# Performance work log

Measured on AMD Instinct MI355X. Metric: run time of the kernel, lower is better.

The kernel has to match this reference:

```python
import jax, jax.numpy as jnp
import numpy as np

VNUM = 50000
OUT = 128
E = 1600000
EPS = 1e-7


def setup_inputs() -> dict:
    key = jax.random.key(0)
    k = jax.random.split(key, 8)
    sidx = jax.random.randint(k[0], (E,), 0, VNUM, dtype=jnp.int64 if jax.config.jax_enable_x64 else jnp.int32)
    tidx = jax.random.randint(k[1], (E,), 0, VNUM, dtype=sidx.dtype)
    enorm = jax.random.uniform(k[2], (E,), dtype=jnp.float32)
    # edge signs +-1 as in signed graph conv
    esgn = jnp.where(jax.random.uniform(k[3], (E,)) < 0.5, -1.0, 1.0).astype(jnp.float32)
    # vrepr initialized trunc_normal(std=0.1) (zero_init=False)
    vrepr = 0.1 * jax.random.truncated_normal(k[4], -2.0, 2.0, (VNUM, OUT), dtype=jnp.float32)
    lim = 1.0 / np.sqrt(OUT)
    loc_w = jax.random.uniform(k[5], (OUT, OUT), jnp.float32, -lim, lim)
    loc_b = jnp.zeros((OUT,), jnp.float32)
    std_w = jax.random.uniform(k[6], (OUT, OUT), jnp.float32, -lim, lim)
    std_b = jnp.zeros((OUT,), jnp.float32)
    return {"sidx": sidx, "tidx": tidx, "enorm": enorm, "esgn": esgn,
            "vrepr": vrepr, "loc_w": loc_w, "loc_b": loc_b,
            "std_w": std_w, "std_b": std_b}


def reference(sidx, tidx, enorm, esgn, vrepr, loc_w, loc_b, std_w, std_b):
    # GraphConv: edge-weighted gather + scatter-add aggregation
    msg = vrepr[sidx] * (esgn * enorm)[:, None]          # [E, OUT]
    ptr = jax.ops.segment_sum(msg, tidx, num_segments=VNUM)  # [VNUM, OUT]
    loc = ptr @ loc_w.T + loc_b                          # Normal loc
    std = jax.nn.softplus(ptr @ std_w.T + std_b) + EPS   # Normal scale
    return loc, std
```

## Files before the change

kernel.cpp:

```cpp
#include <hip/hip_runtime.h>
#include <math.h>

#define VNUM 50000
#define OUTF 128
#define NEDGE 1600000
#define EPSF 1e-7f

#define CONV_BLOCKS 6250
#define BFRAG_BLOCKS 64

#define CHUNK 2048
#define NCB 49
#define COARSE_BLOCKS 782

typedef __attribute__((ext_vector_type(8))) short short8;
typedef __attribute__((ext_vector_type(4))) float v4f;

__device__ __forceinline__ unsigned short f2bf(float f) {
    union { float f; unsigned int u; } c; c.f = f;
    unsigned int u = c.u;
    return (unsigned short)((u + 0x7FFFu + ((u >> 16) & 1u)) >> 16);
}
__device__ __forceinline__ float bf16_lo(unsigned int p) {
    union { unsigned int u; float f; } c; c.u = p << 16; return c.f;
}
__device__ __forceinline__ float bf16_hi(unsigned int p) {
    union { unsigned int u; float f; } c; c.u = p & 0xFFFF0000u; return c.f;
}

__device__ __forceinline__ int wave_incl_scan(int v, int lane) {
#pragma unroll
    for (int off = 1; off < 64; off <<= 1) {
        const int o = __shfl_up(v, off, 64);
        if (lane >= off) v += o;
    }
    return v;
}

__global__ __launch_bounds__(256) void prep_kernel(
    const float* __restrict__ vrepr, unsigned int* __restrict__ vrepr16,
    const int* __restrict__ tidx, int* __restrict__ chist,
    const float* __restrict__ loc_w, const float* __restrict__ std_w,
    unsigned int* bfrag)
{
    __shared__ int lc[4][NCB];
    const int b = blockIdx.x, tid = threadIdx.x;
    if (b < CONV_BLOCKS) {
        const size_t base = (size_t)b * 1024 + tid * 4;
        const float4 v = *reinterpret_cast<const float4*>(vrepr + base);
        uint2 o;
        o.x = (unsigned)f2bf(v.x) | ((unsigned)f2bf(v.y) << 16);
        o.y = (unsigned)f2bf(v.z) | ((unsigned)f2bf(v.w) << 16);
        *reinterpret_cast<uint2*>(vrepr16 + base / 2) = o;
    } else if (b < CONV_BLOCKS + COARSE_BLOCKS) {
        const int hb = b - CONV_BLOCKS;
        for (int i = tid; i < 4 * NCB; i += 256) (&lc[0][0])[i] = 0;
        __syncthreads();
        const int base = hb * CHUNK;
#pragma unroll
        for (int j = 0; j < 8; ++j) {
            const int e = base + j * 256 + tid;
            if (e < NEDGE) atomicAdd(&lc[tid >> 6][tidx[e] >> 10], 1);
        }
        __syncthreads();
        if (tid < NCB) {
            const int s = lc[0][tid] + lc[1][tid] + lc[2][tid] + lc[3][tid];
            if (s) atomicAdd(&chist[tid], s);
        }
    } else {
        const int p = (b - (CONV_BLOCKS + COARSE_BLOCKS)) * 256 + tid;
        const int j2 = p & 3, lq = (p >> 2) & 63, ks = (p >> 8) & 3, ct = p >> 10;
        const int k = ks * 32 + (lq >> 4) * 8 + j2 * 2;
        const int n = ct * 16 + (lq & 15);
        const float* wsrc = (n >> 7) ? std_w : loc_w;
        const int c = n & 127;
        bfrag[p] = (unsigned)f2bf(wsrc[c * 128 + k]) |
                   ((unsigned)f2bf(wsrc[c * 128 + k + 1]) << 16);
    }
}

__global__ __launch_bounds__(64) void scan_coarse_kernel(
    const int* __restrict__ chist, int* __restrict__ cbase,
    int* __restrict__ ccursor, int* __restrict__ offs)
{
    const int tid = threadIdx.x;
    const int v = (tid < NCB) ? chist[tid] : 0;
    const int inc = wave_incl_scan(v, tid);
    const int ex = inc - v;
    if (tid < NCB) { cbase[tid] = ex; ccursor[tid] = ex; }
    if (tid == NCB - 1) { cbase[NCB] = inc; offs[VNUM] = inc; }
}

__global__ __launch_bounds__(256) void coarse_kernel(
    const int* __restrict__ sidx, const int* __restrict__ tidx,
    const float* __restrict__ enorm, const float* __restrict__ esgn,
    int* __restrict__ ccursor, uint2* __restrict__ coarse8)
{
    __shared__ uint2 lrec[CHUNK];
    __shared__ int lcnt[4][NCB];
    __shared__ int lbase[4][NCB];
    __shared__ int loffs[NCB];
    __shared__ int grun[NCB];

    const int tid = threadIdx.x, lane = tid & 63, wv = tid >> 6;
    const int base = blockIdx.x * CHUNK;
    const int n = min(CHUNK, NEDGE - base);

    for (int i = tid; i < 4 * NCB; i += 256) (&lcnt[0][0])[i] = 0;
    __syncthreads();

    uint2 rec[8];
#pragma unroll
    for (int j = 0; j < 8; ++j) {
        const int e = base + j * 256 + tid;
        if (e < NEDGE) {
            const int t = tidx[e];
            const float w = esgn[e] * enorm[e];
            rec[j].x = ((unsigned)sidx[e] << 16) | (unsigned)f2bf(w);
            rec[j].y = (unsigned)t;
            atomicAdd(&lcnt[wv][t >> 10], 1);
        }
    }
    __syncthreads();

    if (tid < 64) {
        int c0 = 0, c1 = 0, c2 = 0, c3 = 0, tot = 0;
        if (lane < NCB) {
            c0 = lcnt[0][lane]; c1 = lcnt[1][lane];
            c2 = lcnt[2][lane]; c3 = lcnt[3][lane];
            tot = c0 + c1 + c2 + c3;
        }
        const int inc = wave_incl_scan(tot, lane);
        const int ex = inc - tot;
        if (lane < NCB) {
            loffs[lane]    = ex;
            lbase[0][lane] = ex;
            lbase[1][lane] = ex + c0;
            lbase[2][lane] = ex + c0 + c1;
            lbase[3][lane] = ex + c0 + c1 + c2;
            grun[lane] = atomicAdd(&ccursor[lane], tot);
        }
    }
    __syncthreads();

#pragma unroll
    for (int j = 0; j < 8; ++j) {
        const int e = base + j * 256 + tid;
        if (e < NEDGE) {
            const int cb = (int)(rec[j].y >> 10);
            const int pos = atomicAdd(&lbase[wv][cb], 1);
            lrec[pos] = rec[j];
        }
    }
    __syncthreads();

    for (int i = tid; i < n; i += 256) {
        const uint2 r = lrec[i];
        const int cb = (int)(r.y >> 10);
        coarse8[grun[cb] + (i - loffs[cb])] = r;
    }
}

__global__ __launch_bounds__(1024) void binsort_kernel(
    const uint2* __restrict__ coarse8, const int* __restrict__ cbase,
    int* __restrict__ offs, unsigned int* __restrict__ pairs)
{
    __shared__ int cnt[1024];
    __shared__ int cur[1024];
    __shared__ int wsum[16];
    const int tid = threadIdx.x, lane = tid & 63, wv = tid >> 6;
    const int bin = blockIdx.x;
    const int s0 = cbase[bin], e0 = cbase[bin + 1];

    cnt[tid] = 0;
    __syncthreads();
    for (int i = s0 + tid; i < e0; i += 1024)
        atomicAdd(&cnt[coarse8[i].y & 1023], 1);
    __syncthreads();

    const int v = cnt[tid];
    const int inc = wave_incl_scan(v, lane);
    if (lane == 63) wsum[wv] = inc;
    __syncthreads();
    if (tid == 0) {
        int run = 0;
        for (int i2 = 0; i2 < 16; ++i2) { const int t2 = wsum[i2]; wsum[i2] = run; run += t2; }
    }
    __syncthreads();
    const int ex = s0 + wsum[wv] + inc - v;
    const int gv = (bin << 10) + tid;
    if (gv < VNUM) offs[gv] = ex;
    cur[tid] = ex;
    __syncthreads();

    for (int i = s0 + tid; i < e0; i += 1024) {
        const uint2 r = coarse8[i];
        const int pos = atomicAdd(&cur[r.y & 1023], 1);
        pairs[pos] = r.x;
    }
}

__global__ __launch_bounds__(256) void aggregate_kernel(
    const int* __restrict__ offs, const unsigned int* __restrict__ pairs,
    const unsigned int* __restrict__ vrepr16, float* __restrict__ acc)
{
    const int v = blockIdx.x * 4 + (threadIdx.x >> 6);
    const int l = threadIdx.x & 63;
    int i = offs[v];
    const int end = offs[v + 1];

    float a0 = 0.0f, a1 = 0.0f;
    for (; i + 8 <= end; i += 8) {
        unsigned p[8], r[8];
#pragma unroll
        for (int j = 0; j < 8; ++j) p[j] = pairs[i + j];
#pragma unroll
        for (int j = 0; j < 8; ++j) r[j] = vrepr16[(size_t)(p[j] >> 16) * 64 + l];
#pragma unroll
        for (int j = 0; j < 8; ++j) {
            const float w = bf16_lo(p[j]);
            a0 = fmaf(bf16_lo(r[j]), w, a0);
            a1 = fmaf(bf16_hi(r[j]), w, a1);
        }
    }
    for (; i + 4 <= end; i += 4) {
        const unsigned p0 = pairs[i], p1 = pairs[i + 1];
        const unsigned p2 = pairs[i + 2], p3 = pairs[i + 3];
        const unsigned r0 = vrepr16[(size_t)(p0 >> 16) * 64 + l];
        const unsigned r1 = vrepr16[(size_t)(p1 >> 16) * 64 + l];
        const unsigned r2 = vrepr16[(size_t)(p2 >> 16) * 64 + l];
        const unsigned r3 = vrepr16[(size_t)(p3 >> 16) * 64 + l];
        const float w0 = bf16_lo(p0), w1 = bf16_lo(p1);
        const float w2 = bf16_lo(p2), w3 = bf16_lo(p3);
        a0 = fmaf(bf16_lo(r0), w0, a0); a1 = fmaf(bf16_hi(r0), w0, a1);
        a0 = fmaf(bf16_lo(r1), w1, a0); a1 = fmaf(bf16_hi(r1), w1, a1);
        a0 = fmaf(bf16_lo(r2), w2, a0); a1 = fmaf(bf16_hi(r2), w2, a1);
        a0 = fmaf(bf16_lo(r3), w3, a0); a1 = fmaf(bf16_hi(r3), w3, a1);
    }
    for (; i < end; ++i) {
        const unsigned p = pairs[i];
        const unsigned r = vrepr16[(size_t)(p >> 16) * 64 + l];
        const float w = bf16_lo(p);
        a0 = fmaf(bf16_lo(r), w, a0); a1 = fmaf(bf16_hi(r), w, a1);
    }
    *reinterpret_cast<float2*>(acc + (size_t)v * OUTF + 2 * l) = make_float2(a0, a1);
}

__global__ __launch_bounds__(256) void gemm_mfma_kernel(
    const float* acc, const unsigned int* __restrict__ bfrag,
    const float* __restrict__ loc_b, const float* __restrict__ std_b,
    float* out)
{
    __shared__ unsigned short tile[16][136];
    const int t = threadIdx.x;
    const int row0 = blockIdx.x * 16;
    const int l = t & 63, w = t >> 6;

    short8 bfr[4][4];
#pragma unroll
    for (int ct = 0; ct < 4; ++ct)
#pragma unroll
        for (int ks = 0; ks < 4; ++ks)
            bfr[ct][ks] = *reinterpret_cast<const short8*>(
                bfrag + ((((w * 4 + ct) * 4 + ks) * 64 + l) << 2));

    {
        const float* src = acc + (size_t)row0 * OUTF + t * 8;
        const float4 v0 = *reinterpret_cast<const float4*>(src);
        const float4 v1 = *reinterpret_cast<const float4*>(src + 4);
        uint4 pk;
        pk.x = (unsigned)f2bf(v0.x) | ((unsigned)f2bf(v0.y) << 16);
        pk.y = (unsigned)f2bf(v0.z) | ((unsigned)f2bf(v0.w) << 16);
        pk.z = (unsigned)f2bf(v1.x) | ((unsigned)f2bf(v1.y) << 16);
        pk.w = (unsigned)f2bf(v1.z) | ((unsigned)f2bf(v1.w) << 16);
        *reinterpret_cast<uint4*>(&tile[t >> 4][(t & 15) * 8]) = pk;
    }
    __syncthreads();

    const int m = l & 15, q = l >> 4;
    v4f accv[4];
#pragma unroll
    for (int ct = 0; ct < 4; ++ct) accv[ct] = (v4f){0.0f, 0.0f, 0.0f, 0.0f};

#pragma unroll
    for (int ks = 0; ks < 4; ++ks) {
        const short8 a = *reinterpret_cast<const short8*>(&tile[m][ks * 32 + q * 8]);
#pragma unroll
        for (int ct = 0; ct < 4; ++ct)
            accv[ct] = __builtin_amdgcn_mfma_f32_16x16x32_bf16(
                a, bfr[ct][ks], accv[ct], 0, 0, 0);
    }

#pragma unroll
    for (int ct = 0; ct < 4; ++ct) {
        const int colg = (w * 4 + ct) * 16 + m;
        const int h = colg >> 7, c = colg & 127;
        const float bias = (h ? std_b : loc_b)[c];
        float* dst = out + (h ? (size_t)VNUM * OUTF : (size_t)0);
#pragma unroll
        for (int reg = 0; reg < 4; ++reg) {
            const int row = row0 + q * 4 + reg;
            float x = accv[ct][reg] + bias;
            if (h) x = fmaxf(x, 0.0f) + log1pf(expf(-fabsf(x))) + EPSF;
            dst[(size_t)row * OUTF + c] = x;
        }
    }
}

__global__ __launch_bounds__(256) void gemm_fallback_kernel(
    const float* acc,
    const float* __restrict__ loc_w, const float* __restrict__ loc_b,
    const float* __restrict__ std_w, const float* __restrict__ std_b,
    float* out)
{
    __shared__ float tile[16][OUTF];
    const int t = threadIdx.x;
    const int row0 = blockIdx.x * 16;
    {
        const float4* src = reinterpret_cast<const float4*>(acc + (size_t)row0 * OUTF);
        float4* dst = reinterpret_cast<float4*>(&tile[0][0]);
        dst[t] = src[t]; dst[t + 256] = src[t + 256];
    }
    __syncthreads();
    const int is_std = t >> 7;
    const int c = t & 127;
    const float* w = (is_std ? std_w : loc_w) + (size_t)c * OUTF;
    const float bias = is_std ? std_b[c] : loc_b[c];
    float accv[16];
#pragma unroll
    for (int r = 0; r < 16; ++r) accv[r] = 0.0f;
    for (int k = 0; k < OUTF; k += 4) {
        const float4 wv = *reinterpret_cast<const float4*>(w + k);
#pragma unroll
        for (int r = 0; r < 16; ++r) {
            const float4 pv = *reinterpret_cast<const float4*>(&tile[r][k]);
            float a = accv[r];
            a = fmaf(pv.x, wv.x, a); a = fmaf(pv.y, wv.y, a);
            a = fmaf(pv.z, wv.z, a); a = fmaf(pv.w, wv.w, a);
            accv[r] = a;
        }
    }
    float* dst_base = out + (is_std ? (size_t)VNUM * OUTF : (size_t)0);
#pragma unroll
    for (int r = 0; r < 16; ++r) {
        const float x = accv[r] + bias;
        dst_base[(size_t)(row0 + r) * OUTF + c] =
            is_std ? (fmaxf(x, 0.0f) + log1pf(expf(-fabsf(x))) + EPSF) : x;
    }
}

extern "C" void kernel_launch(void* const* d_in, const int* in_sizes, int n_in,
                              void* d_out, int out_size, void* d_ws, size_t ws_size,
                              hipStream_t stream) {
    const int*   sidx  = (const int*)  d_in[0];
    const int*   tidx  = (const int*)  d_in[1];
    const float* enorm = (const float*)d_in[2];
    const float* esgn  = (const float*)d_in[3];
    const float* vrepr = (const float*)d_in[4];
    const float* loc_w = (const float*)d_in[5];
    const float* loc_b = (const float*)d_in[6];
    const float* std_w = (const float*)d_in[7];
    const float* std_b = (const float*)d_in[8];

    float* out = (float*)d_out;

    uint2* coarse8 = (uint2*)out;

    unsigned int* sbase   = (unsigned int*)(out + (size_t)VNUM * OUTF);
    unsigned int* pairs   = sbase;
    unsigned int* vrepr16 = sbase + NEDGE;
    int* offs    = (int*)(sbase + NEDGE + (size_t)VNUM * 64);
    int* cbase   = offs + VNUM + 1;
    int* ccursor = cbase + NCB + 1;
    int* chist   = ccursor + NCB;

    const bool use_ws = ws_size >= 16384 * sizeof(unsigned int);
    unsigned int* bfrag = use_ws ? (unsigned int*)d_ws : nullptr;

    hipMemsetAsync(chist, 0, NCB * sizeof(int), stream);

    const int prep_blocks = CONV_BLOCKS + COARSE_BLOCKS + (use_ws ? BFRAG_BLOCKS : 0);
    prep_kernel       <<<prep_blocks, 256, 0, stream>>>(vrepr, vrepr16, tidx, chist,
                                                        loc_w, std_w, bfrag);
    scan_coarse_kernel<<<1, 64, 0, stream>>>(chist, cbase, ccursor, offs);
    coarse_kernel     <<<COARSE_BLOCKS, 256, 0, stream>>>(sidx, tidx, enorm, esgn,
                                                          ccursor, coarse8);
    binsort_kernel    <<<NCB, 1024, 0, stream>>>(coarse8, cbase, offs, pairs);

    float* acc = out;
    aggregate_kernel<<<VNUM / 4, 256, 0, stream>>>(offs, pairs, vrepr16, acc);

    if (use_ws) {
        gemm_mfma_kernel<<<VNUM / 16, 256, 0, stream>>>(acc, bfrag, loc_b, std_b, out);
    } else {
        gemm_fallback_kernel<<<VNUM / 16, 256, 0, stream>>>(acc, loc_w, loc_b,
                                                            std_w, std_b, out);
    }
}
```

Measured before the change: 266.0 us.

## Replace per-bin sort with global fine histogram and XCD-aware atomic scatter

After: 347.2 us. 1.31x slower.

```diff
diff --git a/kernel.cpp b/kernel.cpp
--- a/kernel.cpp
+++ b/kernel.cpp
@@ -12,6 +12,8 @@
 #define CHUNK 2048
 #define NCB 49
 #define COARSE_BLOCKS 782
+#define SC_Q 97
+#define SC_R 6
 
 typedef __attribute__((ext_vector_type(8))) short short8;
 typedef __attribute__((ext_vector_type(4))) float v4f;
@@ -40,6 +42,7 @@
 __global__ __launch_bounds__(256) void prep_kernel(
     const float* __restrict__ vrepr, unsigned int* __restrict__ vrepr16,
     const int* __restrict__ tidx, int* __restrict__ chist,
+    int* __restrict__ fcnt,
     const float* __restrict__ loc_w, const float* __restrict__ std_w,
     unsigned int* bfrag)
 {
@@ -60,7 +63,11 @@
 #pragma unroll
         for (int j = 0; j < 8; ++j) {
             const int e = base + j * 256 + tid;
-            if (e < NEDGE) atomicAdd(&lc[tid >> 6][tidx[e] >> 10], 1);
+            if (e < NEDGE) {
+                const int t = tidx[e];
+                atomicAdd(&lc[tid >> 6][t >> 10], 1);
+                atomicAdd(&fcnt[t], 1);
+            }
         }
         __syncthreads();
         if (tid < NCB) {
@@ -79,16 +86,37 @@
     }
 }
 
-__global__ __launch_bounds__(64) void scan_coarse_kernel(
-    const int* __restrict__ chist, int* __restrict__ cbase,
-    int* __restrict__ ccursor, int* __restrict__ offs)
-{
-    const int tid = threadIdx.x;
-    const int v = (tid < NCB) ? chist[tid] : 0;
-    const int inc = wave_incl_scan(v, tid);
-    const int ex = inc - v;
-    if (tid < NCB) { cbase[tid] = ex; ccursor[tid] = ex; }
-    if (tid == NCB - 1) { cbase[NCB] = inc; offs[VNUM] = inc; }
+__global__ __launch_bounds__(1024) void scan_fine_kernel(
+    const int* __restrict__ chist, const int* __restrict__ fcnt,
+    int* __restrict__ ccursor, int* __restrict__ offs,
+    int* __restrict__ gcur)
+{
+    __shared__ int wsum[16];
+    __shared__ int cbs;
+    const int tid = threadIdx.x, lane = tid & 63, wv = tid >> 6;
+    const int bin = blockIdx.x;
+
+    if (tid < 64) {
+        int c = (tid < bin) ? chist[tid] : 0;
+#pragma unroll
+        for (int off = 32; off; off >>= 1) c += __shfl_xor(c, off, 64);
+        if (tid == 0) { cbs = c; ccursor[bin] = c; }
+    }
+    __syncthreads();
+
+    const int gv = (bin << 10) + tid;
+    const int v = fcnt[gv];
+    const int inc = wave_incl_scan(v, lane);
+    if (lane == 63) wsum[wv] = inc;
+    __syncthreads();
+    if (tid == 0) {
+        int run = 0;
+        for (int i = 0; i < 16; ++i) { const int t = wsum[i]; wsum[i] = run; run += t; }
+    }
+    __syncthreads();
+    const int ex = cbs + wsum[wv] + inc - v;
+    if (gv < VNUM) { offs[gv] = ex; gcur[gv] = ex; }
+    if (bin == NCB - 1 && tid == 1023) offs[VNUM] = ex + v;
 }
 
 __global__ __launch_bounds__(256) void coarse_kernel(
@@ -161,42 +189,24 @@
     }
 }
 
-__global__ __launch_bounds__(1024) void binsort_kernel(
-    const uint2* __restrict__ coarse8, const int* __restrict__ cbase,
-    int* __restrict__ offs, unsigned int* __restrict__ pairs)
-{
-    __shared__ int cnt[1024];
-    __shared__ int cur[1024];
-    __shared__ int wsum[16];
-    const int tid = threadIdx.x, lane = tid & 63, wv = tid >> 6;
-    const int bin = blockIdx.x;
-    const int s0 = cbase[bin], e0 = cbase[bin + 1];
-
-    cnt[tid] = 0;
-    __syncthreads();
-    for (int i = s0 + tid; i < e0; i += 1024)
-        atomicAdd(&cnt[coarse8[i].y & 1023], 1);
-    __syncthreads();
-
-    const int v = cnt[tid];
-    const int inc = wave_incl_scan(v, lane);
-    if (lane == 63) wsum[wv] = inc;
-    __syncthreads();
-    if (tid == 0) {
-        int run = 0;
-        for (int i2 = 0; i2 < 16; ++i2) { const int t2 = wsum[i2]; wsum[i2] = run; run += t2; }
-    }
-    __syncthreads();
-    const int ex = s0 + wsum[wv] + inc - v;
-    const int gv = (bin << 10) + tid;
-    if (gv < VNUM) offs[gv] = ex;
-    cur[tid] = ex;
-    __syncthreads();
-
-    for (int i = s0 + tid; i < e0; i += 1024) {
-        const uint2 r = coarse8[i];
-        const int pos = atomicAdd(&cur[r.y & 1023], 1);
-        pairs[pos] = r.x;
+__global__ __launch_bounds__(256) void scatter_kernel(
+    const uint2* __restrict__ coarse8, int* __restrict__ gcur,
+    unsigned int* __restrict__ pairs)
+{
+    const int o = blockIdx.x;
+    const int xcd = o & 7;
+    const int wg = (xcd < SC_R ? xcd * (SC_Q + 1)
+                               : SC_R * (SC_Q + 1) + (xcd - SC_R) * SC_Q) + (o >> 3);
+    const int tid = threadIdx.x;
+    const int base = wg * CHUNK;
+#pragma unroll
+    for (int j = 0; j < 8; ++j) {
+        const int e = base + j * 256 + tid;
+        if (e < NEDGE) {
+            const uint2 r = coarse8[e];
+            const int pos = atomicAdd(&gcur[r.y], 1);
+            pairs[pos] = r.x;
+        }
     }
 }
 
@@ -370,22 +380,23 @@
     unsigned int* pairs   = sbase;
     unsigned int* vrepr16 = sbase + NEDGE;
     int* offs    = (int*)(sbase + NEDGE + (size_t)VNUM * 64);
-    int* cbase   = offs + VNUM + 1;
-    int* ccursor = cbase + NCB + 1;
+    int* ccursor = offs + VNUM + 1;
     int* chist   = ccursor + NCB;
+    int* fcnt    = chist + NCB;
+    int* gcur    = fcnt + NCB * 1024;
 
     const bool use_ws = ws_size >= 16384 * sizeof(unsigned int);
     unsigned int* bfrag = use_ws ? (unsigned int*)d_ws : nullptr;
 
-    hipMemsetAsync(chist, 0, NCB * sizeof(int), stream);
+    hipMemsetAsync(chist, 0, (NCB + NCB * 1024) * sizeof(int), stream);
 
     const int prep_blocks = CONV_BLOCKS + COARSE_BLOCKS + (use_ws ? BFRAG_BLOCKS : 0);
-    prep_kernel       <<<prep_blocks, 256, 0, stream>>>(vrepr, vrepr16, tidx, chist,
-                                                        loc_w, std_w, bfrag);
-    scan_coarse_kernel<<<1, 64, 0, stream>>>(chist, cbase, ccursor, offs);
-    coarse_kernel     <<<COARSE_BLOCKS, 256, 0, stream>>>(sidx, tidx, enorm, esgn,
-                                                          ccursor, coarse8);
-    binsort_kernel    <<<NCB, 1024, 0, stream>>>(coarse8, cbase, offs, pairs);
+    prep_kernel     <<<prep_blocks, 256, 0, stream>>>(vrepr, vrepr16, tidx, chist,
+                                                      fcnt, loc_w, std_w, bfrag);
+    scan_fine_kernel<<<NCB, 1024, 0, stream>>>(chist, fcnt, ccursor, offs, gcur);
+    coarse_kernel   <<<COARSE_BLOCKS, 256, 0, stream>>>(sidx, tidx, enorm, esgn,
+                                                        ccursor, coarse8);
+    scatter_kernel  <<<COARSE_BLOCKS, 256, 0, stream>>>(coarse8, gcur, pairs);
 
     float* acc = out;
     aggregate_kernel<<<VNUM / 4, 256, 0, stream>>>(offs, pairs, vrepr16, acc);
```

## Split per-bin fine sort into four sub-blocks with separate histogram pass

Applied to the files above, without the earlier changes.

New measurement: 253.3 us. -4.8%, faster.

```diff
diff --git a/kernel.cpp b/kernel.cpp
--- a/kernel.cpp
+++ b/kernel.cpp
@@ -12,6 +12,8 @@
 #define CHUNK 2048
 #define NCB 49
 #define COARSE_BLOCKS 782
+#define NSUB 4
+#define FINE_BLOCKS (NCB * NSUB)
 
 typedef __attribute__((ext_vector_type(8))) short short8;
 typedef __attribute__((ext_vector_type(4))) float v4f;
@@ -161,39 +163,59 @@
     }
 }
 
-__global__ __launch_bounds__(1024) void binsort_kernel(
+__global__ __launch_bounds__(1024) void hist_kernel(
     const uint2* __restrict__ coarse8, const int* __restrict__ cbase,
-    int* __restrict__ offs, unsigned int* __restrict__ pairs)
+    int* __restrict__ hcnt)
 {
     __shared__ int cnt[1024];
+    const int tid = threadIdx.x;
+    const int bin = blockIdx.x >> 2, s = blockIdx.x & 3;
+    const int s0 = cbase[bin], len = cbase[bin + 1] - s0;
+    const int qs = s0 + ((len * s) >> 2);
+    const int qe = s0 + ((len * (s + 1)) >> 2);
+    cnt[tid] = 0;
+    __syncthreads();
+    for (int i = qs + tid; i < qe; i += 1024)
+        atomicAdd(&cnt[coarse8[i].y & 1023], 1);
+    __syncthreads();
+    hcnt[blockIdx.x * 1024 + tid] = cnt[tid];
+}
+
+__global__ __launch_bounds__(1024) void scatter_fine_kernel(
+    const uint2* __restrict__ coarse8, const int* __restrict__ cbase,
+    const int* __restrict__ hcnt, int* __restrict__ offs,
+    unsigned int* __restrict__ pairs)
+{
     __shared__ int cur[1024];
     __shared__ int wsum[16];
     const int tid = threadIdx.x, lane = tid & 63, wv = tid >> 6;
-    const int bin = blockIdx.x;
-    const int s0 = cbase[bin], e0 = cbase[bin + 1];
-
-    cnt[tid] = 0;
-    __syncthreads();
-    for (int i = s0 + tid; i < e0; i += 1024)
-        atomicAdd(&cnt[coarse8[i].y & 1023], 1);
-    __syncthreads();
-
-    const int v = cnt[tid];
-    const int inc = wave_incl_scan(v, lane);
+    const int bin = blockIdx.x >> 2, s = blockIdx.x & 3;
+    const int s0 = cbase[bin], len = cbase[bin + 1] - s0;
+    const int qs = s0 + ((len * s) >> 2);
+    const int qe = s0 + ((len * (s + 1)) >> 2);
+
+    const int c0 = hcnt[(bin * 4 + 0) * 1024 + tid];
+    const int c1 = hcnt[(bin * 4 + 1) * 1024 + tid];
+    const int c2 = hcnt[(bin * 4 + 2) * 1024 + tid];
+    const int c3 = hcnt[(bin * 4 + 3) * 1024 + tid];
+    const int tot = c0 + c1 + c2 + c3;
+    const int pre = (s > 0 ? c0 : 0) + (s > 1 ? c1 : 0) + (s > 2 ? c2 : 0);
+
+    const int inc = wave_incl_scan(tot, lane);
     if (lane == 63) wsum[wv] = inc;
     __syncthreads();
     if (tid == 0) {
         int run = 0;
-        for (int i2 = 0; i2 < 16; ++i2) { const int t2 = wsum[i2]; wsum[i2] = run; run += t2; }
-    }
-    __syncthreads();
-    const int ex = s0 + wsum[wv] + inc - v;
+        for (int i = 0; i < 16; ++i) { const int t = wsum[i]; wsum[i] = run; run += t; }
+    }
+    __syncthreads();
+    const int ex = s0 + wsum[wv] + inc - tot;
     const int gv = (bin << 10) + tid;
-    if (gv < VNUM) offs[gv] = ex;
-    cur[tid] = ex;
-    __syncthreads();
-
-    for (int i = s0 + tid; i < e0; i += 1024) {
+    if (s == 0 && gv < VNUM) offs[gv] = ex;
+    cur[tid] = ex + pre;
+    __syncthreads();
+
+    for (int i = qs + tid; i < qe; i += 1024) {
         const uint2 r = coarse8[i];
         const int pos = atomicAdd(&cur[r.y & 1023], 1);
         pairs[pos] = r.x;
@@ -373,6 +395,7 @@
     int* cbase   = offs + VNUM + 1;
     int* ccursor = cbase + NCB + 1;
     int* chist   = ccursor + NCB;
+    int* hcnt    = chist + NCB;
 
     const bool use_ws = ws_size >= 16384 * sizeof(unsigned int);
     unsigned int* bfrag = use_ws ? (unsigned int*)d_ws : nullptr;
@@ -385,7 +408,9 @@
     scan_coarse_kernel<<<1, 64, 0, stream>>>(chist, cbase, ccursor, offs);
     coarse_kernel     <<<COARSE_BLOCKS, 256, 0, stream>>>(sidx, tidx, enorm, esgn,
                                                           ccursor, coarse8);
-    binsort_kernel    <<<NCB, 1024, 0, stream>>>(coarse8, cbase, offs, pairs);
+    hist_kernel       <<<FINE_BLOCKS, 1024, 0, stream>>>(coarse8, cbase, hcnt);
+    scatter_fine_kernel<<<FINE_BLOCKS, 1024, 0, stream>>>(coarse8, cbase, hcnt,
+                                                          offs, pairs);
 
     float* acc = out;
     aggregate_kernel<<<VNUM / 4, 256, 0, stream>>>(offs, pairs, vrepr16, acc);
```
